# Kernel optimization log

Hardware: AMD Instinct MI355X
Metric: run time of the kernel (lower is better)

## Reference

```python
import jax, jax.numpy as jnp
import numpy as np

N = 50000
E = 800000
F_IN = 128


def _gat(h, src, dst, W, a_src, a_dst, bias, heads, out_ch, concat):
    n = h.shape[0]
    z = (h @ W.T).reshape(n, heads, out_ch)              # [N,H,C]
    alpha_s = jnp.sum(z * a_src, axis=-1)                # [N,H]
    alpha_d = jnp.sum(z * a_dst, axis=-1)                # [N,H]
    logits = jax.nn.leaky_relu(alpha_s[src] + alpha_d[dst], 0.2)  # [Etot,H]
    m = jax.ops.segment_max(logits, dst, num_segments=n)
    ex = jnp.exp(logits - m[dst])
    denom = jax.ops.segment_sum(ex, dst, num_segments=n)
    w = ex / (denom[dst] + 1e-16)                        # [Etot,H]
    agg = jax.ops.segment_sum(w[:, :, None] * z[src], dst, num_segments=n)  # [N,H,C]
    if concat:
        out = agg.reshape(n, heads * out_ch)
    else:
        out = agg.mean(axis=1)
    return out + bias


def setup_inputs() -> dict:
    key = jax.random.key(0)
    ks = jax.random.split(key, 16)
    s = lambda *sh: 1.0 / np.sqrt(sh[-1])
    inp = {
        "x": jax.random.normal(ks[0], (N, F_IN), jnp.float32),
        "edge_index": jax.random.randint(ks[1], (2, E), 0, N, jnp.int64),
        # GraphConv(no_node_features=128 -> 128, aggr='add')
        "W_rel": jax.random.normal(ks[2], (128, F_IN), jnp.float32) * s(128, F_IN),
        "b_rel": jnp.zeros((128,), jnp.float32),
        "W_root": jax.random.normal(ks[3], (128, F_IN), jnp.float32) * s(128, F_IN),
        # GATConv(128 -> 8, heads=8, concat) => 64
        "W1": jax.random.normal(ks[4], (64, 128), jnp.float32) * s(64, 128),
        "a1_src": jax.random.normal(ks[5], (8, 8), jnp.float32) * 0.35,
        "a1_dst": jax.random.normal(ks[6], (8, 8), jnp.float32) * 0.35,
        "b1": jnp.zeros((64,), jnp.float32),
        # GATConv(64 -> 64, heads=1, concat=False)
        "W2": jax.random.normal(ks[7], (64, 64), jnp.float32) * s(64, 64),
        "a2_src": jax.random.normal(ks[8], (1, 64), jnp.float32) * 0.125,
        "a2_dst": jax.random.normal(ks[9], (1, 64), jnp.float32) * 0.125,
        "b2": jnp.zeros((64,), jnp.float32),
        "Wr": jax.random.normal(ks[10], (1, 64), jnp.float32) * s(1, 64),
        "br": jnp.zeros((1,), jnp.float32),
    }
    return inp


def reference(x, edge_index, W_rel, b_rel, W_root, W1, a1_src, a1_dst, b1,
              W2, a2_src, a2_dst, b2, Wr, br):
    src, dst = edge_index[0], edge_index[1]
    # GraphConv, aggr='add': W_rel @ sum_{j in N(i)} x_j + b + W_root @ x_i
    nbr = jax.ops.segment_sum(x[src], dst, num_segments=N)
    h = nbr @ W_rel.T + b_rel + x @ W_root.T
    h = jax.nn.elu(h)
    # GATConv adds self-loops by default
    loop = jnp.arange(N, dtype=edge_index.dtype)
    src2 = jnp.concatenate([src, loop])
    dst2 = jnp.concatenate([dst, loop])
    h = _gat(h, src2, dst2, W1, a1_src, a1_dst, b1, heads=8, out_ch=8, concat=True)
    h = jax.nn.elu(h)
    h = _gat(h, src2, dst2, W2, a2_src, a2_dst, b2, heads=1, out_ch=64, concat=False)
    # final 'mean' aggregation over all nodes (single graph)
    g = jnp.mean(h, axis=0, keepdims=True)               # [1,64]
    return g @ Wr.T + br                                  # [1,1]
```

## Files before the change

kernel.cpp:

```cpp
#include <hip/hip_runtime.h>
#include <hip/hip_bf16.h>
#include <math.h>

#define N_NODES 50000
#define N_EDGES 800000
#define F_IN 128
#define NBUCK 391
#define EPB 4096
#define NBB 196

typedef __attribute__((ext_vector_type(8))) short bf16x8;
typedef __attribute__((ext_vector_type(4))) float f32x4;
typedef __attribute__((ext_vector_type(2))) float f32x2;
typedef unsigned long long ull;

__device__ __forceinline__ float elu_f(float x)   { return x > 0.f ? x : expm1f(x); }
__device__ __forceinline__ float lrelu_f(float x) { return x > 0.f ? x : 0.2f * x; }
__device__ __forceinline__ int   clampN(int v)    { return v < 0 ? 0 : (v >= N_NODES ? N_NODES - 1 : v); }
__device__ __forceinline__ float bits2f(unsigned int u) { union { unsigned int u; float f; } x; x.u = u; return x.f; }
__device__ __forceinline__ float lo16(unsigned int u) { return bits2f(u << 16); }
__device__ __forceinline__ float hi16(unsigned int u) { return bits2f(u & 0xffff0000u); }
__device__ __forceinline__ unsigned short f2bfbits(float f) {
    __hip_bfloat16 b = __float2bfloat16(f);
    return __builtin_bit_cast(unsigned short, b);
}
__device__ __forceinline__ unsigned int pack2(float lo, float hi) {
    return ((unsigned int)f2bfbits(hi) << 16) | f2bfbits(lo);
}

__global__ __launch_bounds__(256) void k_bhist(const int* __restrict__ dst,
                                               int* __restrict__ bcount) {
    __shared__ int hist[NBUCK];
    int tid = threadIdx.x;
    for (int j = tid; j < NBUCK; j += 256) hist[j] = 0;
    __syncthreads();
    int base = blockIdx.x * EPB;
    #pragma unroll
    for (int t = 0; t < EPB / 256; ++t) {
        int e = base + t * 256 + tid;
        if (e < N_EDGES) atomicAdd(&hist[clampN(dst[e]) >> 7], 1);
    }
    __syncthreads();
    for (int j = tid; j < NBUCK; j += 256)
        if (hist[j]) atomicAdd(&bcount[j], hist[j]);
}

__global__ __launch_bounds__(512) void k_bscan(const int* __restrict__ bcount,
                                               int* __restrict__ boff,
                                               int* __restrict__ bcur) {
    __shared__ int wsum[8];
    __shared__ int wbase[8];
    int tid = threadIdx.x;
    int lane = tid & 63, wid = tid >> 6;
    int v = (tid < NBUCK) ? bcount[tid] : 0;
    int x = v;
    #pragma unroll
    for (int d = 1; d < 64; d <<= 1) {
        int t = __shfl_up(x, d, 64);
        if (lane >= d) x += t;
    }
    if (lane == 63) wsum[wid] = x;
    __syncthreads();
    if (tid == 0) {
        int b = 0;
        #pragma unroll
        for (int w = 0; w < 8; ++w) { wbase[w] = b; b += wsum[w]; }
    }
    __syncthreads();
    if (tid < NBUCK) {
        int e = wbase[wid] + x - v;
        boff[tid] = e;
        bcur[tid] = e;
    }
    if (tid == 0) boff[NBUCK] = N_EDGES;
}

__global__ __launch_bounds__(256) void k_bscatter(const int* __restrict__ src,
                                                  const int* __restrict__ dst,
                                                  int* __restrict__ bcur,
                                                  int2* __restrict__ ebuf) {
    __shared__ int hist[NBUCK];
    __shared__ int hbase[NBUCK];
    int tid = threadIdx.x;
    for (int j = tid; j < NBUCK; j += 256) hist[j] = 0;
    __syncthreads();
    int base = blockIdx.x * EPB;
    int myS[EPB / 256], myD[EPB / 256], myR[EPB / 256];
    #pragma unroll
    for (int t = 0; t < EPB / 256; ++t) {
        int e = base + t * 256 + tid;
        if (e < N_EDGES) {
            int d = clampN(dst[e]);
            myS[t] = clampN(src[e]);
            myD[t] = d;
            myR[t] = atomicAdd(&hist[d >> 7], 1);
        } else myD[t] = -1;
    }
    __syncthreads();
    for (int j = tid; j < NBUCK; j += 256)
        if (hist[j]) hbase[j] = atomicAdd(&bcur[j], hist[j]);
    __syncthreads();
    #pragma unroll
    for (int t = 0; t < EPB / 256; ++t) {
        if (myD[t] >= 0) {
            int b = myD[t] >> 7;
            ebuf[hbase[b] + myR[t]] = make_int2(myS[t], myD[t]);
        }
    }
}

__global__ __launch_bounds__(256) void k_bfinal(const int2* __restrict__ ebuf,
                                                const int* __restrict__ boff,
                                                int* __restrict__ offsets,
                                                int* __restrict__ csr) {
    __shared__ int cnt[128];
    __shared__ int cur[128];
    __shared__ int ws[4];
    int b = blockIdx.x;
    int tid = threadIdx.x;
    int node0 = b << 7;
    int k0 = boff[b], k1 = boff[b + 1];
    if (tid < 128) cnt[tid] = 0;
    __syncthreads();
    for (int k = k0 + tid; k < k1; k += 256)
        atomicAdd(&cnt[ebuf[k].y & 127], 1);
    __syncthreads();
    int lane = tid & 63;
    int v = (tid < 128) ? cnt[tid] : 0;
    int x = v;
    #pragma unroll
    for (int d = 1; d < 64; d <<= 1) {
        int t = __shfl_up(x, d, 64);
        if (lane >= d) x += t;
    }
    if (lane == 63) ws[tid >> 6] = x;
    __syncthreads();
    if (tid < 128) {
        int add = (tid >> 6) ? ws[0] : 0;
        int excl = k0 + add + x - v;
        cur[tid] = excl;
        int node = node0 + tid;
        if (node < N_NODES) offsets[node] = excl;
    }
    if (b == NBUCK - 1 && tid == 0) offsets[N_NODES] = N_EDGES;
    __syncthreads();
    for (int k = k0 + tid; k < k1; k += 256) {
        int2 e = ebuf[k];
        int r = atomicAdd(&cur[e.y & 127], 1);
        csr[r] = e.x;
    }
}

#define CAST_X_IDS (N_NODES * 32)
__global__ void k_cast(const float* __restrict__ x,
                       const float* __restrict__ W_rel, const float* __restrict__ W_root,
                       const float* __restrict__ W1, const float* __restrict__ W2,
                       __hip_bfloat16* __restrict__ Abuf, __hip_bfloat16* __restrict__ Wc,
                       __hip_bfloat16* __restrict__ W1b, __hip_bfloat16* __restrict__ W2b) {
    int id = blockIdx.x * 256 + threadIdx.x;
    if (id < CAST_X_IDS) {
        int i = id >> 5, c4 = (id & 31) * 4;
        float4 v = *(const float4*)&x[(size_t)i * 128 + c4];
        ull p = (ull)f2bfbits(v.x) | ((ull)f2bfbits(v.y) << 16)
              | ((ull)f2bfbits(v.z) << 32) | ((ull)f2bfbits(v.w) << 48);
        *(ull*)&Abuf[(size_t)i * 256 + 128 + c4] = p;
    } else {
        int j = id - CAST_X_IDS;
        if (j < 32768) {
            int cc = j >> 8, k = j & 255;
            float v = (k < 128) ? W_rel[cc * 128 + k] : W_root[cc * 128 + (k - 128)];
            Wc[j] = __float2bfloat16(v);
        } else if (j < 32768 + 8192) {
            W1b[j - 32768] = __float2bfloat16(W1[j - 32768]);
        } else if (j < 32768 + 8192 + 4096) {
            W2b[j - 32768 - 8192] = __float2bfloat16(W2[j - 32768 - 8192]);
        }
    }
}

__global__ __launch_bounds__(256) void k_gather(const unsigned int* __restrict__ A,
                                                const int* __restrict__ offsets,
                                                const int* __restrict__ csr,
                                                unsigned int* __restrict__ out) {
    int i = blockIdx.x * 8 + (threadIdx.x >> 5);
    int l = threadIdx.x & 31;
    int k0 = offsets[i], k1 = offsets[i + 1];
    float a0 = 0.f, a1 = 0.f, b0 = 0.f, b1v = 0.f;
    for (int kb = k0; kb < k1; kb += 8) {
        int   s[8];
        int   vmask[8];
        #pragma unroll
        for (int j = 0; j < 8; ++j) {
            int kk = kb + j;
            vmask[j] = kk < k1;
            s[j] = csr[vmask[j] ? kk : k1 - 1];
        }
        unsigned int ua[8], va[8];
        #pragma unroll
        for (int j = 0; j < 8; ++j) {
            ua[j] = A[(size_t)s[j] * 128 + 64 + l];
            va[j] = A[(size_t)s[j] * 128 + 96 + l];
        }
        #pragma unroll
        for (int j = 0; j < 8; ++j) {
            if (vmask[j]) {
                a0  += lo16(ua[j]); a1  += hi16(ua[j]);
                b0  += lo16(va[j]); b1v += hi16(va[j]);
            }
        }
    }
    out[(size_t)i * 128 + l]      = pack2(a0, a1);
    out[(size_t)i * 128 + 32 + l] = pack2(b0, b1v);
}

template<int K, int N, bool ELU, bool BIAS>
__global__ __launch_bounds__(256) void k_gemm(const __hip_bfloat16* __restrict__ A,
                                              const __hip_bfloat16* __restrict__ W,
                                              const float* __restrict__ bias,
                                              __hip_bfloat16* __restrict__ Out) {
    constexpr int NT = N / 16;
    __shared__ __align__(16) short sA[64][40];
    __shared__ __align__(16) short sW[N][40];
    int tid = threadIdx.x;
    int lane = tid & 63, wave = tid >> 6;
    int quad = lane >> 4, l16 = lane & 15;
    int node0 = blockIdx.x * 64;
    int srow = tid >> 2, schk = (tid & 3) * 8;
    int ga = node0 + srow; if (ga >= N_NODES) ga = N_NODES - 1;
    const short* Ap = (const short*)A + (size_t)ga * K + schk;
    const short* Wp = (const short*)W;
    f32x4 acc[NT];
    #pragma unroll
    for (int t = 0; t < NT; ++t) acc[t] = (f32x4){0.f, 0.f, 0.f, 0.f};
    for (int k0 = 0; k0 < K; k0 += 32) {
        *(bf16x8*)&sA[srow][schk] = *(const bf16x8*)(Ap + k0);
        #pragma unroll
        for (int it = 0; it < N / 64; ++it) {
            int wrow = srow + it * 64;
            *(bf16x8*)&sW[wrow][schk] = *(const bf16x8*)(Wp + (size_t)wrow * K + k0 + schk);
        }
        __syncthreads();
        bf16x8 a = *(const bf16x8*)&sA[wave * 16 + l16][quad * 8];
        #pragma unroll
        for (int nt = 0; nt < NT; ++nt) {
            bf16x8 b = *(const bf16x8*)&sW[nt * 16 + l16][quad * 8];
            acc[nt] = __builtin_amdgcn_mfma_f32_16x16x32_bf16(a, b, acc[nt], 0, 0, 0);
        }
        __syncthreads();
    }
    int mbase = node0 + wave * 16 + quad * 4;
    #pragma unroll
    for (int nt = 0; nt < NT; ++nt) {
        int col = nt * 16 + l16;
        float bv = BIAS ? bias[col] : 0.f;
        #pragma unroll
        for (int r = 0; r < 4; ++r) {
            int m = mbase + r;
            if (m < N_NODES) {
                float v = acc[nt][r] + bv;
                if (ELU) v = elu_f(v);
                Out[(size_t)m * N + col] = __float2bfloat16(v);
            }
        }
    }
}

__global__ __launch_bounds__(256) void k_alpha1(const __hip_bfloat16* __restrict__ z1,
                                                const float* __restrict__ a_src,
                                                const float* __restrict__ a_dst,
                                                float* __restrict__ as1, float* __restrict__ ad1,
                                                unsigned int* __restrict__ z8) {
    int i = blockIdx.x * 4 + (threadIdx.x >> 6);
    if (i >= N_NODES) return;
    int c = threadIdx.x & 63;
    float v = __bfloat162float(z1[(size_t)i * 64 + c]);
    float ps = v * a_src[c];
    float pd = v * a_dst[c];
    #pragma unroll
    for (int d = 4; d >= 1; d >>= 1) {
        ps += __shfl_down(ps, d, 8);
        pd += __shfl_down(pd, d, 8);
    }
    if ((c & 7) == 0) {
        as1[(size_t)i * 8 + (c >> 3)] = ps;
        ad1[(size_t)i * 8 + (c >> 3)] = pd;
    }
    float vn = __shfl_down(v, 1, 64);
    unsigned int pk = (unsigned int)__builtin_amdgcn_cvt_pk_fp8_f32(v, vn, 0, false);
    unsigned int pk2 = __shfl_down(pk, 2, 64);
    if ((c & 3) == 0) z8[(size_t)i * 16 + (c >> 2)] = (pk & 0xffffu) | (pk2 << 16);
}

__global__ __launch_bounds__(256) void k_alpha2(const __hip_bfloat16* __restrict__ z2,
                                                const float* __restrict__ a_src,
                                                const float* __restrict__ a_dst,
                                                float* __restrict__ as2, float* __restrict__ ad2,
                                                unsigned int* __restrict__ z8) {
    int i = blockIdx.x * 4 + (threadIdx.x >> 6);
    if (i >= N_NODES) return;
    int c = threadIdx.x & 63;
    float v = __bfloat162float(z2[(size_t)i * 64 + c]);
    float ps = v * a_src[c];
    float pd = v * a_dst[c];
    #pragma unroll
    for (int d = 32; d >= 1; d >>= 1) {
        ps += __shfl_down(ps, d, 64);
        pd += __shfl_down(pd, d, 64);
    }
    if (c == 0) { as2[i] = ps; ad2[i] = pd; }
    float vn = __shfl_down(v, 1, 64);
    unsigned int pk = (unsigned int)__builtin_amdgcn_cvt_pk_fp8_f32(v, vn, 0, false);
    unsigned int pk2 = __shfl_down(pk, 2, 64);
    if ((c & 3) == 0) z8[(size_t)i * 16 + (c >> 2)] = (pk & 0xffffu) | (pk2 << 16);
}

__global__ __launch_bounds__(256) void k_gat1attn(const unsigned int* __restrict__ z8,
                                                  const float* __restrict__ as1,
                                                  const float* __restrict__ ad1,
                                                  const float* __restrict__ b1,
                                                  const int* __restrict__ offsets,
                                                  const int* __restrict__ csr,
                                                  ull* __restrict__ h2u) {
    int i = blockIdx.x * 16 + (threadIdx.x >> 4);
    int l = threadIdx.x & 15;
    int hd = l >> 1;
    int wh = l & 7, slot = l >> 3;
    int k0 = offsets[i], k1 = offsets[i + 1];
    float ad_h = ad1[(size_t)i * 8 + hd];
    float adw  = ad1[(size_t)i * 8 + wh];
    float e_self = __expf(lrelu_f(as1[(size_t)i * 8 + hd] + ad_h));
    unsigned int uz = z8[(size_t)i * 16 + l];
    f32x2 zlo = __builtin_amdgcn_cvt_pk_f32_fp8(uz, false);
    f32x2 zhi = __builtin_amdgcn_cvt_pk_f32_fp8(uz, true);
    float acc0 = e_self * zlo.x, acc1 = e_self * zlo.y;
    float acc2 = e_self * zhi.x, acc3 = e_self * zhi.y;
    float denp = 0.f;
    for (int kb = k0; kb < k1; kb += 4) {
        int ka = kb + slot, kc = kb + 2 + slot;
        bool va = ka < k1, vb = kc < k1;
        int sa = csr[va ? ka : k1 - 1];
        int sb = csr[vb ? kc : k1 - 1];
        float ea = va ? __expf(lrelu_f(as1[(size_t)sa * 8 + wh] + adw)) : 0.f;
        float eb = vb ? __expf(lrelu_f(as1[(size_t)sb * 8 + wh] + adw)) : 0.f;
        denp += ea + eb;
        int sj[4]; float ej[4];
        #pragma unroll
        for (int j = 0; j < 2; ++j) {
            sj[j]     = __shfl(sa, j * 8 + hd, 16);
            ej[j]     = __shfl(ea, j * 8 + hd, 16);
            sj[2 + j] = __shfl(sb, j * 8 + hd, 16);
            ej[2 + j] = __shfl(eb, j * 8 + hd, 16);
        }
        unsigned int u[4];
        #pragma unroll
        for (int j = 0; j < 4; ++j) u[j] = z8[(size_t)sj[j] * 16 + l];
        #pragma unroll
        for (int j = 0; j < 4; ++j) {
            f32x2 alo = __builtin_amdgcn_cvt_pk_f32_fp8(u[j], false);
            f32x2 ahi = __builtin_amdgcn_cvt_pk_f32_fp8(u[j], true);
            acc0 += ej[j] * alo.x; acc1 += ej[j] * alo.y;
            acc2 += ej[j] * ahi.x; acc3 += ej[j] * ahi.y;
        }
    }
    denp += __shfl_xor(denp, 8, 16);
    float den = __shfl(denp, hd, 16) + e_self;
    float inv = 1.f / den;
    float r0 = elu_f(acc0 * inv + b1[4 * l + 0]);
    float r1 = elu_f(acc1 * inv + b1[4 * l + 1]);
    float r2 = elu_f(acc2 * inv + b1[4 * l + 2]);
    float r3 = elu_f(acc3 * inv + b1[4 * l + 3]);
    h2u[(size_t)i * 16 + l] = (ull)pack2(r0, r1) | ((ull)pack2(r2, r3) << 32);
}

__global__ __launch_bounds__(256) void k_gat2attn(const unsigned int* __restrict__ z8,
                                                  const float* __restrict__ as2,
                                                  const float* __restrict__ ad2,
                                                  const float* __restrict__ b2,
                                                  const int* __restrict__ offsets,
                                                  const int* __restrict__ csr,
                                                  const float* __restrict__ Wr,
                                                  float* __restrict__ red) {
    int i = blockIdx.x * 16 + (threadIdx.x >> 4);
    int l = threadIdx.x & 15;
    int k0 = offsets[i], k1 = offsets[i + 1];
    float ad = ad2[i];
    float e_self = __expf(lrelu_f(as2[i] + ad));
    unsigned int uz = z8[(size_t)i * 16 + l];
    f32x2 zlo = __builtin_amdgcn_cvt_pk_f32_fp8(uz, false);
    f32x2 zhi = __builtin_amdgcn_cvt_pk_f32_fp8(uz, true);
    float acc0 = e_self * zlo.x, acc1 = e_self * zlo.y;
    float acc2 = e_self * zhi.x, acc3 = e_self * zhi.y;
    float denp = (l == 0) ? e_self : 0.f;
    for (int kb = k0; kb < k1; kb += 16) {
        int kk = kb + l;
        bool v = kk < k1;
        int s = csr[v ? kk : k1 - 1];
        float e = v ? __expf(lrelu_f(as2[s] + ad)) : 0.f;
        denp += e;
        int nv = k1 - kb; if (nv > 16) nv = 16;
        for (int j0 = 0; j0 < nv; j0 += 4) {
            int sj[4]; float ej[4]; unsigned int u[4];
            #pragma unroll
            for (int j = 0; j < 4; ++j) {
                int idx = (j0 + j) & 15;
                sj[j] = __shfl(s, idx, 16);
                ej[j] = __shfl(e, idx, 16);
            }
            #pragma unroll
            for (int j = 0; j < 4; ++j) u[j] = z8[(size_t)sj[j] * 16 + l];
            #pragma unroll
            for (int j = 0; j < 4; ++j) {
                f32x2 alo = __builtin_amdgcn_cvt_pk_f32_fp8(u[j], false);
                f32x2 ahi = __builtin_amdgcn_cvt_pk_f32_fp8(u[j], true);
                acc0 += ej[j] * alo.x; acc1 += ej[j] * alo.y;
                acc2 += ej[j] * ahi.x; acc3 += ej[j] * ahi.y;
            }
        }
    }
    #pragma unroll
    for (int d = 8; d >= 1; d >>= 1) denp += __shfl_xor(denp, d, 16);
    float inv = 1.f / denp;
    float c = (acc0 * inv + b2[4 * l + 0]) * Wr[4 * l + 0]
            + (acc1 * inv + b2[4 * l + 1]) * Wr[4 * l + 1]
            + (acc2 * inv + b2[4 * l + 2]) * Wr[4 * l + 2]
            + (acc3 * inv + b2[4 * l + 3]) * Wr[4 * l + 3];
    #pragma unroll
    for (int d = 8; d >= 1; d >>= 1) c += __shfl_xor(c, d, 16);
    if (l == 0) atomicAdd(&red[blockIdx.x & 255], c);
}

__global__ void k_finalize(const float* __restrict__ red, const float* __restrict__ br,
                           float* __restrict__ out) {
    int t = threadIdx.x;
    float s = red[t] + red[t + 64] + red[t + 128] + red[t + 192];
    #pragma unroll
    for (int d = 32; d >= 1; d >>= 1) s += __shfl_xor(s, d, 64);
    if (t == 0) out[0] = s * (1.0f / N_NODES) + br[0];
}

extern "C" void kernel_launch(void* const* d_in, const int* in_sizes, int n_in,
                              void* d_out, int out_size, void* d_ws, size_t ws_size,
                              hipStream_t stream) {
    const float* x      = (const float*)d_in[0];
    const int*   edges  = (const int*)d_in[1];
    const float* W_rel  = (const float*)d_in[2];
    const float* b_rel  = (const float*)d_in[3];
    const float* W_root = (const float*)d_in[4];
    const float* W1     = (const float*)d_in[5];
    const float* a1s    = (const float*)d_in[6];
    const float* a1d    = (const float*)d_in[7];
    const float* b1     = (const float*)d_in[8];
    const float* W2     = (const float*)d_in[9];
    const float* a2s    = (const float*)d_in[10];
    const float* a2d    = (const float*)d_in[11];
    const float* b2     = (const float*)d_in[12];
    const float* Wr     = (const float*)d_in[13];
    const float* br     = (const float*)d_in[14];
    float* out = (float*)d_out;

    const int* src = edges;
    const int* dst = edges + N_EDGES;

    char* ws = (char*)d_ws;
    size_t p = 0;
    auto alloc = [&](size_t bytes) -> void* {
        void* r = ws + p;
        p = (p + bytes + 255) & ~(size_t)255;
        return r;
    };
    int*   bcount  = (int*)alloc((size_t)NBUCK * 4);
    int*   boff    = (int*)alloc((size_t)(NBUCK + 1) * 4);
    int*   bcur    = (int*)alloc((size_t)NBUCK * 4);
    int2*  ebuf    = (int2*)alloc((size_t)N_EDGES * 8);
    int*   offsets = (int*)alloc((size_t)(N_NODES + 1) * 4);
    int*   csr     = (int*)alloc((size_t)N_EDGES * 4);
    __hip_bfloat16* Abuf = (__hip_bfloat16*)alloc((size_t)N_NODES * 256 * 2);
    __hip_bfloat16* Wc   = (__hip_bfloat16*)alloc((size_t)128 * 256 * 2);
    __hip_bfloat16* W1b  = (__hip_bfloat16*)alloc((size_t)64 * 128 * 2);
    __hip_bfloat16* W2b  = (__hip_bfloat16*)alloc((size_t)64 * 64 * 2);
    __hip_bfloat16* h    = (__hip_bfloat16*)alloc((size_t)N_NODES * 128 * 2);
    __hip_bfloat16* z1b  = (__hip_bfloat16*)alloc((size_t)N_NODES * 64 * 2);
    float* as1 = (float*)alloc((size_t)N_NODES * 8 * 4);
    float* ad1 = (float*)alloc((size_t)N_NODES * 8 * 4);
    __hip_bfloat16* h2b  = (__hip_bfloat16*)alloc((size_t)N_NODES * 64 * 2);
    __hip_bfloat16* z2b  = (__hip_bfloat16*)alloc((size_t)N_NODES * 64 * 2);
    float* as2 = (float*)alloc((size_t)N_NODES * 4);
    float* ad2 = (float*)alloc((size_t)N_NODES * 4);
    unsigned int* z1e8 = (unsigned int*)alloc((size_t)N_NODES * 16 * 4);
    unsigned int* z2e8 = (unsigned int*)alloc((size_t)N_NODES * 16 * 4);
    float* red = (float*)alloc(256 * 4);

    hipMemsetAsync(bcount, 0, (size_t)NBUCK * 4, stream);
    hipMemsetAsync(red, 0, 256 * 4, stream);

    const int MB   = (N_NODES + 63) / 64;
    const int NB4  = (N_NODES + 3) / 4;
    const int NB8  = N_NODES / 8;
    const int NB16 = N_NODES / 16;
    const int CAST_IDS = CAST_X_IDS + 32768 + 8192 + 4096;

    k_bhist   <<<NBB, 256, 0, stream>>>(dst, bcount);
    k_bscan   <<<1, 512, 0, stream>>>(bcount, boff, bcur);
    k_bscatter<<<NBB, 256, 0, stream>>>(src, dst, bcur, ebuf);
    k_bfinal  <<<NBUCK, 256, 0, stream>>>(ebuf, boff, offsets, csr);
    k_cast    <<<(CAST_IDS + 255) / 256, 256, 0, stream>>>(x, W_rel, W_root, W1, W2, Abuf, Wc, W1b, W2b);
    k_gather  <<<NB8, 256, 0, stream>>>((const unsigned int*)Abuf, offsets, csr, (unsigned int*)Abuf);
    k_gemm<256, 128, true,  true ><<<MB, 256, 0, stream>>>(Abuf, Wc, b_rel, h);
    k_gemm<128, 64,  false, false><<<MB, 256, 0, stream>>>(h, W1b, nullptr, z1b);
    k_alpha1  <<<NB4, 256, 0, stream>>>(z1b, a1s, a1d, as1, ad1, z1e8);
    k_gat1attn<<<NB16, 256, 0, stream>>>(z1e8, as1, ad1, b1, offsets, csr, (ull*)h2b);
    k_gemm<64, 64, false, false><<<MB, 256, 0, stream>>>(h2b, W2b, nullptr, z2b);
    k_alpha2  <<<NB4, 256, 0, stream>>>(z2b, a2s, a2d, as2, ad2, z2e8);
    k_gat2attn<<<NB16, 256, 0, stream>>>(z2e8, as2, ad2, b2, offsets, csr, Wr, red);
    k_finalize<<<1, 64, 0, stream>>>(red, br, out);
}
```

Measured before the change: 266.9 us.

## Gather neighbor features in fp8, pack edge buffer, widen attention unroll

```diff
diff --git a/kernel.cpp b/kernel.cpp
--- a/kernel.cpp
+++ b/kernel.cpp
@@ -78,23 +78,24 @@
 __global__ __launch_bounds__(256) void k_bscatter(const int* __restrict__ src,
                                                   const int* __restrict__ dst,
                                                   int* __restrict__ bcur,
-                                                  int2* __restrict__ ebuf) {
+                                                  unsigned int* __restrict__ ebuf) {
     __shared__ int hist[NBUCK];
     __shared__ int hbase[NBUCK];
     int tid = threadIdx.x;
     for (int j = tid; j < NBUCK; j += 256) hist[j] = 0;
     __syncthreads();
     int base = blockIdx.x * EPB;
-    int myS[EPB / 256], myD[EPB / 256], myR[EPB / 256];
+    unsigned int myP[EPB / 256]; int myB[EPB / 256], myR[EPB / 256];
     #pragma unroll
     for (int t = 0; t < EPB / 256; ++t) {
         int e = base + t * 256 + tid;
         if (e < N_EDGES) {
             int d = clampN(dst[e]);
-            myS[t] = clampN(src[e]);
-            myD[t] = d;
+            int s = clampN(src[e]);
+            myP[t] = ((unsigned int)s << 7) | (unsigned int)(d & 127);
+            myB[t] = d >> 7;
             myR[t] = atomicAdd(&hist[d >> 7], 1);
-        } else myD[t] = -1;
+        } else myB[t] = -1;
     }
     __syncthreads();
     for (int j = tid; j < NBUCK; j += 256)
@@ -102,14 +103,11 @@
     __syncthreads();
     #pragma unroll
     for (int t = 0; t < EPB / 256; ++t) {
-        if (myD[t] >= 0) {
-            int b = myD[t] >> 7;
-            ebuf[hbase[b] + myR[t]] = make_int2(myS[t], myD[t]);
-        }
-    }
-}
-
-__global__ __launch_bounds__(256) void k_bfinal(const int2* __restrict__ ebuf,
+        if (myB[t] >= 0) ebuf[hbase[myB[t]] + myR[t]] = myP[t];
+    }
+}
+
+__global__ __launch_bounds__(256) void k_bfinal(const unsigned int* __restrict__ ebuf,
                                                 const int* __restrict__ boff,
                                                 int* __restrict__ offsets,
                                                 int* __restrict__ csr) {
@@ -123,7 +121,7 @@
     if (tid < 128) cnt[tid] = 0;
     __syncthreads();
     for (int k = k0 + tid; k < k1; k += 256)
-        atomicAdd(&cnt[ebuf[k].y & 127], 1);
+        atomicAdd(&cnt[ebuf[k] & 127u], 1);
     __syncthreads();
     int lane = tid & 63;
     int v = (tid < 128) ? cnt[tid] : 0;
@@ -145,9 +143,9 @@
     if (b == NBUCK - 1 && tid == 0) offsets[N_NODES] = N_EDGES;
     __syncthreads();
     for (int k = k0 + tid; k < k1; k += 256) {
-        int2 e = ebuf[k];
-        int r = atomicAdd(&cur[e.y & 127], 1);
-        csr[r] = e.x;
+        unsigned int e = ebuf[k];
+        int r = atomicAdd(&cur[e & 127u], 1);
+        csr[r] = (int)(e >> 7);
     }
 }
 
@@ -155,7 +153,8 @@
 __global__ void k_cast(const float* __restrict__ x,
                        const float* __restrict__ W_rel, const float* __restrict__ W_root,
                        const float* __restrict__ W1, const float* __restrict__ W2,
-                       __hip_bfloat16* __restrict__ Abuf, __hip_bfloat16* __restrict__ Wc,
+                       __hip_bfloat16* __restrict__ Abuf, unsigned int* __restrict__ x8,
+                       __hip_bfloat16* __restrict__ Wc,
                        __hip_bfloat16* __restrict__ W1b, __hip_bfloat16* __restrict__ W2b) {
     int id = blockIdx.x * 256 + threadIdx.x;
     if (id < CAST_X_IDS) {
@@ -164,6 +163,9 @@
         ull p = (ull)f2bfbits(v.x) | ((ull)f2bfbits(v.y) << 16)
               | ((ull)f2bfbits(v.z) << 32) | ((ull)f2bfbits(v.w) << 48);
         *(ull*)&Abuf[(size_t)i * 256 + 128 + c4] = p;
+        int t = __builtin_amdgcn_cvt_pk_fp8_f32(v.x, v.y, 0, false);
+        t = __builtin_amdgcn_cvt_pk_fp8_f32(v.z, v.w, t, true);
+        x8[(size_t)i * 32 + (id & 31)] = (unsigned int)t;
     } else {
         int j = id - CAST_X_IDS;
         if (j < 32768) {
@@ -178,39 +180,35 @@
     }
 }
 
-__global__ __launch_bounds__(256) void k_gather(const unsigned int* __restrict__ A,
+__global__ __launch_bounds__(256) void k_gather(const unsigned int* __restrict__ x8,
                                                 const int* __restrict__ offsets,
                                                 const int* __restrict__ csr,
-                                                unsigned int* __restrict__ out) {
+                                                ull* __restrict__ outNbr) {
     int i = blockIdx.x * 8 + (threadIdx.x >> 5);
     int l = threadIdx.x & 31;
     int k0 = offsets[i], k1 = offsets[i + 1];
-    float a0 = 0.f, a1 = 0.f, b0 = 0.f, b1v = 0.f;
+    float a0 = 0.f, a1 = 0.f, a2 = 0.f, a3 = 0.f;
     for (int kb = k0; kb < k1; kb += 8) {
-        int   s[8];
-        int   vmask[8];
+        int s[8]; int vm[8];
         #pragma unroll
         for (int j = 0; j < 8; ++j) {
             int kk = kb + j;
-            vmask[j] = kk < k1;
-            s[j] = csr[vmask[j] ? kk : k1 - 1];
-        }
-        unsigned int ua[8], va[8];
+            vm[j] = kk < k1;
+            s[j] = csr[vm[j] ? kk : k1 - 1];
+        }
+        unsigned int u[8];
+        #pragma unroll
+        for (int j = 0; j < 8; ++j) u[j] = x8[(size_t)s[j] * 32 + l];
         #pragma unroll
         for (int j = 0; j < 8; ++j) {
-            ua[j] = A[(size_t)s[j] * 128 + 64 + l];
-            va[j] = A[(size_t)s[j] * 128 + 96 + l];
-        }
-        #pragma unroll
-        for (int j = 0; j < 8; ++j) {
-            if (vmask[j]) {
-                a0  += lo16(ua[j]); a1  += hi16(ua[j]);
-                b0  += lo16(va[j]); b1v += hi16(va[j]);
+            if (vm[j]) {
+                f32x2 lo = __builtin_amdgcn_cvt_pk_f32_fp8(u[j], false);
+                f32x2 hi = __builtin_amdgcn_cvt_pk_f32_fp8(u[j], true);
+                a0 += lo.x; a1 += lo.y; a2 += hi.x; a3 += hi.y;
             }
         }
     }
-    out[(size_t)i * 128 + l]      = pack2(a0, a1);
-    out[(size_t)i * 128 + 32 + l] = pack2(b0, b1v);
+    outNbr[(size_t)i * 64 + l] = (ull)pack2(a0, a1) | ((ull)pack2(a2, a3) << 32);
 }
 
 template<int K, int N, bool ELU, bool BIAS>
@@ -335,27 +333,30 @@
     float acc0 = e_self * zlo.x, acc1 = e_self * zlo.y;
     float acc2 = e_self * zhi.x, acc3 = e_self * zhi.y;
     float denp = 0.f;
-    for (int kb = k0; kb < k1; kb += 4) {
-        int ka = kb + slot, kc = kb + 2 + slot;
-        bool va = ka < k1, vb = kc < k1;
-        int sa = csr[va ? ka : k1 - 1];
-        int sb = csr[vb ? kc : k1 - 1];
-        float ea = va ? __expf(lrelu_f(as1[(size_t)sa * 8 + wh] + adw)) : 0.f;
-        float eb = vb ? __expf(lrelu_f(as1[(size_t)sb * 8 + wh] + adw)) : 0.f;
-        denp += ea + eb;
-        int sj[4]; float ej[4];
-        #pragma unroll
-        for (int j = 0; j < 2; ++j) {
-            sj[j]     = __shfl(sa, j * 8 + hd, 16);
-            ej[j]     = __shfl(ea, j * 8 + hd, 16);
-            sj[2 + j] = __shfl(sb, j * 8 + hd, 16);
-            ej[2 + j] = __shfl(eb, j * 8 + hd, 16);
-        }
-        unsigned int u[4];
-        #pragma unroll
-        for (int j = 0; j < 4; ++j) u[j] = z8[(size_t)sj[j] * 16 + l];
-        #pragma unroll
-        for (int j = 0; j < 4; ++j) {
+    for (int kb = k0; kb < k1; kb += 8) {
+        int sr[4]; float er[4];
+        #pragma unroll
+        for (int m = 0; m < 4; ++m) {
+            int kk = kb + 2 * m + slot;
+            bool v = kk < k1;
+            int s = csr[v ? kk : k1 - 1];
+            sr[m] = s;
+            er[m] = v ? __expf(lrelu_f(as1[(size_t)s * 8 + wh] + adw)) : 0.f;
+            denp += er[m];
+        }
+        int sj[8]; float ej[8]; unsigned int u[8];
+        #pragma unroll
+        for (int m = 0; m < 4; ++m) {
+            #pragma unroll
+            for (int sb = 0; sb < 2; ++sb) {
+                sj[2 * m + sb] = __shfl(sr[m], sb * 8 + hd, 16);
+                ej[2 * m + sb] = __shfl(er[m], sb * 8 + hd, 16);
+            }
+        }
+        #pragma unroll
+        for (int j = 0; j < 8; ++j) u[j] = z8[(size_t)sj[j] * 16 + l];
+        #pragma unroll
+        for (int j = 0; j < 8; ++j) {
             f32x2 alo = __builtin_amdgcn_cvt_pk_f32_fp8(u[j], false);
             f32x2 ahi = __builtin_amdgcn_cvt_pk_f32_fp8(u[j], true);
             acc0 += ej[j] * alo.x; acc1 += ej[j] * alo.y;
@@ -398,18 +399,18 @@
         float e = v ? __expf(lrelu_f(as2[s] + ad)) : 0.f;
         denp += e;
         int nv = k1 - kb; if (nv > 16) nv = 16;
-        for (int j0 = 0; j0 < nv; j0 += 4) {
-            int sj[4]; float ej[4]; unsigned int u[4];
+        for (int j0 = 0; j0 < nv; j0 += 8) {
+            int sj[8]; float ej[8]; unsigned int u[8];
             #pragma unroll
-            for (int j = 0; j < 4; ++j) {
+            for (int j = 0; j < 8; ++j) {
                 int idx = (j0 + j) & 15;
                 sj[j] = __shfl(s, idx, 16);
                 ej[j] = __shfl(e, idx, 16);
             }
             #pragma unroll
-            for (int j = 0; j < 4; ++j) u[j] = z8[(size_t)sj[j] * 16 + l];
+            for (int j = 0; j < 8; ++j) u[j] = z8[(size_t)sj[j] * 16 + l];
             #pragma unroll
-            for (int j = 0; j < 4; ++j) {
+            for (int j = 0; j < 8; ++j) {
                 f32x2 alo = __builtin_amdgcn_cvt_pk_f32_fp8(u[j], false);
                 f32x2 ahi = __builtin_amdgcn_cvt_pk_f32_fp8(u[j], true);
                 acc0 += ej[j] * alo.x; acc1 += ej[j] * alo.y;
@@ -471,10 +472,11 @@
     int*   bcount  = (int*)alloc((size_t)NBUCK * 4);
     int*   boff    = (int*)alloc((size_t)(NBUCK + 1) * 4);
     int*   bcur    = (int*)alloc((size_t)NBUCK * 4);
-    int2*  ebuf    = (int2*)alloc((size_t)N_EDGES * 8);
+    unsigned int* ebuf = (unsigned int*)alloc((size_t)N_EDGES * 4);
     int*   offsets = (int*)alloc((size_t)(N_NODES + 1) * 4);
     int*   csr     = (int*)alloc((size_t)N_EDGES * 4);
     __hip_bfloat16* Abuf = (__hip_bfloat16*)alloc((size_t)N_NODES * 256 * 2);
+    unsigned int* x8 = (unsigned int*)alloc((size_t)N_NODES * 32 * 4);
     __hip_bfloat16* Wc   = (__hip_bfloat16*)alloc((size_t)128 * 256 * 2);
     __hip_bfloat16* W1b  = (__hip_bfloat16*)alloc((size_t)64 * 128 * 2);
     __hip_bfloat16* W2b  = (__hip_bfloat16*)alloc((size_t)64 * 64 * 2);
@@ -503,8 +505,8 @@
     k_bscan   <<<1, 512, 0, stream>>>(bcount, boff, bcur);
     k_bscatter<<<NBB, 256, 0, stream>>>(src, dst, bcur, ebuf);
     k_bfinal  <<<NBUCK, 256, 0, stream>>>(ebuf, boff, offsets, csr);
-    k_cast    <<<(CAST_IDS + 255) / 256, 256, 0, stream>>>(x, W_rel, W_root, W1, W2, Abuf, Wc, W1b, W2b);
-    k_gather  <<<NB8, 256, 0, stream>>>((const unsigned int*)Abuf, offsets, csr, (unsigned int*)Abuf);
+    k_cast    <<<(CAST_IDS + 255) / 256, 256, 0, stream>>>(x, W_rel, W_root, W1, W2, Abuf, x8, Wc, W1b, W2b);
+    k_gather  <<<NB8, 256, 0, stream>>>(x8, offsets, csr, (ull*)Abuf);
     k_gemm<256, 128, true,  true ><<<MB, 256, 0, stream>>>(Abuf, Wc, b_rel, h);
     k_gemm<128, 64,  false, false><<<MB, 256, 0, stream>>>(h, W1b, nullptr, z1b);
     k_alpha1  <<<NB4, 256, 0, stream>>>(z1b, a1s, a1d, as1, ad1, z1e8);
```

New measurement: 264.6 us. About the same (-0.9%).
